# Optimization experiments

Measured on AMD Instinct MI355X. Metric: run time of the kernel, lower is better.

Reference implementation:

```python
import jax, jax.numpy as jnp
import numpy as np

K = 16  # nsample for knn_point

def _bn(x, g, b):
    # inference-mode BatchNorm1d folded to per-channel affine (running stats 0/1)
    return x * g[None, :, None] + b[None, :, None]

def _knn(xyz, k):
    # xyz: [B,3,N] -> idx [B,N,k] of k nearest neighbors (squared L2)
    p = xyz.transpose(0, 2, 1)                                   # [B,N,3]
    sq = jnp.sum(p * p, axis=-1)                                 # [B,N]
    d = sq[:, :, None] + sq[:, None, :] - 2.0 * jnp.einsum('bnc,bmc->bnm', p, p)
    _, idx = jax.lax.top_k(-d, k)
    return idx

def _gather(hT, idx):
    # hT: [B,N,C], idx: [B,N,K] -> [B,N,K,C]
    return jax.vmap(lambda a, i: a[i])(hT, idx)

def setup_inputs():
    key = jax.random.key(0)
    ks = jax.random.split(key, 12)
    B, N, C = 16, 2048, 128
    def w(k, shape, fan):
        return jax.random.normal(k, shape, jnp.float32) * (1.0 / np.sqrt(fan))
    o = jnp.ones; z = jnp.zeros
    return {
        'points': jax.random.normal(ks[0], (B, 6, N), jnp.float32),
        'label': jax.random.uniform(ks[1], (B, 1, 16), jnp.float32),
        'We1': w(ks[2], (C, 6), 6), 'ge1': o(C), 'be1': z(C),
        'We2': w(ks[3], (C, C), C), 'ge2': o(C), 'be2': z(C),
        'W1': w(ks[4], (3, C, C), C), 'g1': o((3, C)), 'b1': z((3, C)),
        'W2': w(ks[5], (3, C, C), C), 'g2': o((3, C)), 'b2': z((3, C)),
        'Wf': w(ks[6], (1024, 3 * C), 3 * C), 'gf': o(1024), 'bf': z(1024),
        'Wl': w(ks[7], (64, 16), 16), 'gl': o(64), 'bl': z(64),
        'Wc1': w(ks[8], (512, 3136), 3136), 'bc1': z(512), 'gc1': o(512), 'bb1': z(512),
        'Wc2': w(ks[9], (256, 512), 512), 'bc2': z(256), 'gc2': o(256), 'bb2': z(256),
        'Wc3': w(ks[10], (50, 256), 256), 'bc3': z(50),
    }

def reference(points, label, We1, ge1, be1, We2, ge2, be2, W1, g1, b1, W2, g2, b2,
              Wf, gf, bf, Wl, gl, bl, Wc1, bc1, gc1, bb1, Wc2, bc2, gc2, bb2, Wc3, bc3):
    B, _, N = points.shape
    x = points[:, :6, :]
    xyz = x[:, :3, :]
    idx = _knn(xyz, K)                                            # [B,N,16]
    # input embedding: two conv1x1 + BN + ReLU
    h = jax.nn.relu(_bn(jnp.einsum('oc,bcn->bon', We1, x), ge1, be1))
    h = jax.nn.relu(_bn(jnp.einsum('oc,bcn->bon', We2, h), ge2, be2))
    xs = []
    for i in range(3):  # PVDSA_Res blocks (simplified: conv-BN-ReLU, kNN max-agg, conv-BN + residual)
        t = jax.nn.relu(_bn(jnp.einsum('oc,bcn->bon', W1[i], h), g1[i], b1[i]))
        nbr = _gather(t.transpose(0, 2, 1), idx)                  # [B,N,K,C]
        m = nbr.max(axis=2).transpose(0, 2, 1)                    # [B,C,N]
        h = jax.nn.relu(_bn(jnp.einsum('oc,bcn->bon', W2[i], m), g2[i], b2[i]) + h)
        xs.append(h)
    xcat = jnp.concatenate(xs, axis=1)                            # [B,384,N]
    xf = jax.nn.leaky_relu(_bn(jnp.einsum('oc,bcn->bon', Wf, xcat), gf, bf), 0.2)  # [B,1024,N]
    x_max = xf.max(axis=-1)                                       # [B,1024]
    x_avg = xf.mean(axis=-1)                                      # [B,1024]
    cls = jnp.broadcast_to(label.transpose(0, 2, 1), (B, 16, N))
    lab = jax.nn.leaky_relu(_bn(jnp.einsum('oc,bcn->bon', Wl, cls), gl, bl), 0.2)  # [B,64,N]
    glob = jnp.concatenate([
        jnp.broadcast_to(x_max[:, :, None], (B, 1024, N)),
        jnp.broadcast_to(x_avg[:, :, None], (B, 1024, N)),
        lab], axis=1)
    xa = jnp.concatenate([xf, glob], axis=1)                      # [B,3136,N]
    c = jax.nn.relu(_bn(jnp.einsum('oc,bcn->bon', Wc1, xa) + bc1[None, :, None], gc1, bb1))
    c = jax.nn.relu(_bn(jnp.einsum('oc,bcn->bon', Wc2, c) + bc2[None, :, None], gc2, bb2))
    out = jnp.einsum('oc,bcn->bon', Wc3, c) + bc3[None, :, None]  # [B,50,N]
    return out
```

## Files before the change

kernel.cpp:

```cpp
#include <hip/hip_runtime.h>
#include <cstdint>
#include <cstddef>

#define DEVINL __device__ __forceinline__

typedef float    f32x4 __attribute__((ext_vector_type(4)));
typedef _Float16 f16x8 __attribute__((ext_vector_type(8)));
typedef _Float16 f16x4 __attribute__((ext_vector_type(4)));
typedef short    s16x8 __attribute__((ext_vector_type(8)));

constexpr int BB = 16, NN = 2048, MM = 32768;

constexpr size_t OFF_WE1 = 0;
constexpr size_t OFF_WE2 = OFF_WE1 + 128 * 64 * 2;
constexpr size_t OFF_W1  = OFF_WE2 + 128 * 128 * 2;
constexpr size_t OFF_W2  = OFF_W1  + 3 * 128 * 128 * 2;
constexpr size_t OFF_WF  = OFF_W2  + 3 * 128 * 128 * 2;
constexpr size_t OFF_WC1 = OFF_WF  + 1024 * 384 * 2;
constexpr size_t OFF_WC2 = OFF_WC1 + 512 * 1024 * 2;
constexpr size_t OFF_WC3 = OFF_WC2 + 256 * 512 * 2;
constexpr size_t OFF_BC2 = OFF_WC3 + 128 * 256 * 2;
constexpr size_t OFF_BC3 = OFF_BC2 + 256 * 4;
constexpr size_t OFF_CVEC= OFF_BC3 + 128 * 4;
constexpr size_t OFF_PMAX= OFF_CVEC+ 16 * 512 * 4;
constexpr size_t OFF_PSUM= OFF_PMAX+ 16 * 16 * 1024 * 4;
constexpr size_t OFF_IDX = OFF_PSUM+ 16 * 16 * 1024 * 4;
constexpr size_t OFF_R1  = 8ull << 20;
constexpr size_t OFF_X0  = OFF_R1;
constexpr size_t OFF_HT  = OFF_R1 + (4ull  << 20);
constexpr size_t OFF_TT  = OFF_R1 + (12ull << 20);
constexpr size_t OFF_MT  = OFF_R1 + (20ull << 20);
constexpr size_t OFF_C1  = OFF_R1;
constexpr size_t OFF_XCAT= OFF_R1 + (32ull << 20);
constexpr size_t OFF_C2  = OFF_XCAT;
constexpr size_t OFF_XF  = OFF_XCAT + (24ull << 20);

__global__ __launch_bounds__(256) void fold_all_kernel(
    const float* We1, const float* ge1, const float* We2, const float* ge2,
    const float* W1,  const float* g1,  const float* W2,  const float* g2,
    const float* Wf,  const float* gf,  const float* Wc1, const float* gc1,
    const float* Wc2, const float* gc2, const float* Wc3,
    const float* gc2b, const float* bc2, const float* bb2, const float* bc3,
    const float* pts, char* ws)
{
    const int bid = blockIdx.x;
    const int tid = threadIdx.x;

    if (bid == 4704) {
        ((float*)(ws + OFF_BC2))[tid] = gc2b[tid] * bc2[tid] + bb2[tid];
        return;
    }
    if (bid == 4705) {
        if (tid < 128) ((float*)(ws + OFF_BC3))[tid] = (tid < 50) ? bc3[tid] : 0.f;
        return;
    }
    if (bid >= 4706) {
        int m = (bid - 4706) * 256 + tid;
        int b = m >> 11, n = m & 2047;
        const float* ps = pts + (size_t)b * 6 * 2048 + n;
        _Float16 tmp[64];
#pragma unroll
        for (int c = 0; c < 64; ++c) tmp[c] = (_Float16)0.f;
#pragma unroll
        for (int c = 0; c < 6; ++c) tmp[c] = (_Float16)ps[(size_t)c << 11];
        _Float16* dst = (_Float16*)(ws + OFF_X0) + (size_t)m * 64;
#pragma unroll
        for (int v = 0; v < 8; ++v) *(f16x8*)(dst + v * 8) = *(const f16x8*)(tmp + v * 8);
        return;
    }

    int id, base;
    if      (bid < 32)   { id = 0;  base = 0;    }
    else if (bid < 96)   { id = 1;  base = 32;   }
    else if (bid < 160)  { id = 2;  base = 96;   }
    else if (bid < 224)  { id = 3;  base = 160;  }
    else if (bid < 288)  { id = 4;  base = 224;  }
    else if (bid < 352)  { id = 5;  base = 288;  }
    else if (bid < 416)  { id = 6;  base = 352;  }
    else if (bid < 480)  { id = 7;  base = 416;  }
    else if (bid < 2016) { id = 8;  base = 480;  }
    else if (bid < 4064) { id = 9;  base = 2016; }
    else if (bid < 4576) { id = 10; base = 4064; }
    else                 { id = 11; base = 4576; }

    const float* src = nullptr; const float* g = nullptr; _Float16* dst = nullptr;
    int O = 0, K = 0, lds = 0, Kp = 0;
    switch (id) {
        case 0:  src = We1; g = ge1; O = 128; K = 6;    lds = 6;    Kp = 64;   dst = (_Float16*)(ws + OFF_WE1); break;
        case 1:  src = We2; g = ge2; O = 128; K = 128;  lds = 128;  Kp = 128;  dst = (_Float16*)(ws + OFF_WE2); break;
        case 2: case 3: case 4: {
            int i = id - 2;
            src = W1 + (size_t)i * 16384; g = g1 + i * 128; O = 128; K = 128; lds = 128; Kp = 128;
            dst = (_Float16*)(ws + OFF_W1) + (size_t)i * 16384; break; }
        case 5: case 6: case 7: {
            int i = id - 5;
            src = W2 + (size_t)i * 16384; g = g2 + i * 128; O = 128; K = 128; lds = 128; Kp = 128;
            dst = (_Float16*)(ws + OFF_W2) + (size_t)i * 16384; break; }
        case 8:  src = Wf;  g = gf;  O = 1024; K = 384;  lds = 384;  Kp = 384;  dst = (_Float16*)(ws + OFF_WF);  break;
        case 9:  src = Wc1; g = gc1; O = 512;  K = 1024; lds = 3136; Kp = 1024; dst = (_Float16*)(ws + OFF_WC1); break;
        case 10: src = Wc2; g = gc2; O = 256;  K = 512;  lds = 512;  Kp = 512;  dst = (_Float16*)(ws + OFF_WC2); break;
        default: src = Wc3; g = nullptr; O = 50; K = 256; lds = 256; Kp = 256;  dst = (_Float16*)(ws + OFF_WC3); break;
    }
    int e = (bid - base) * 256 + tid;
    int o = e / Kp, k = e - o * Kp;
    float v = 0.f;
    if (o < O && k < K) {
        v = src[(size_t)o * lds + k];
        if (g) v *= g[o];
    }
    dst[e] = (_Float16)v;
}

DEVINL float knn_dist(const float4 pq, const float4 pm) {
    float t = pq.x * pm.x;
    t = fmaf(pq.y, pm.y, t);
    t = fmaf(pq.z, pm.z, t);
    return fmaf(-2.f, t, pm.w);
}

#define KNN_DINS(X) do { \
    const float x_ = (X); \
    d15 = __builtin_amdgcn_fmed3f(x_, d14, d15); \
    d14 = __builtin_amdgcn_fmed3f(x_, d13, d14); \
    d13 = __builtin_amdgcn_fmed3f(x_, d12, d13); \
    d12 = __builtin_amdgcn_fmed3f(x_, d11, d12); \
    d11 = __builtin_amdgcn_fmed3f(x_, d10, d11); \
    d10 = __builtin_amdgcn_fmed3f(x_, d9,  d10); \
    d9  = __builtin_amdgcn_fmed3f(x_, d8,  d9);  \
    d8  = __builtin_amdgcn_fmed3f(x_, d7,  d8);  \
    d7  = __builtin_amdgcn_fmed3f(x_, d6,  d7);  \
    d6  = __builtin_amdgcn_fmed3f(x_, d5,  d6);  \
    d5  = __builtin_amdgcn_fmed3f(x_, d4,  d5);  \
    d4  = __builtin_amdgcn_fmed3f(x_, d3,  d4);  \
    d3  = __builtin_amdgcn_fmed3f(x_, d2,  d3);  \
    d2  = __builtin_amdgcn_fmed3f(x_, d1,  d2);  \
    d1  = __builtin_amdgcn_fmed3f(x_, d0,  d1);  \
    d0  = __builtin_amdgcn_fmed3f(x_, -3.4e38f, d0); \
} while (0)

#define KNN_CE(A, B) { const float lo_ = fminf(A, B), hi_ = fmaxf(A, B); A = lo_; B = hi_; }

#define KNN_MERGE(OFF) do { \
    const float n0  = __shfl_xor(d0,  OFF), n1  = __shfl_xor(d1,  OFF), \
                n2  = __shfl_xor(d2,  OFF), n3  = __shfl_xor(d3,  OFF), \
                n4  = __shfl_xor(d4,  OFF), n5  = __shfl_xor(d5,  OFF), \
                n6  = __shfl_xor(d6,  OFF), n7  = __shfl_xor(d7,  OFF), \
                n8  = __shfl_xor(d8,  OFF), n9  = __shfl_xor(d9,  OFF), \
                n10 = __shfl_xor(d10, OFF), n11 = __shfl_xor(d11, OFF), \
                n12 = __shfl_xor(d12, OFF), n13 = __shfl_xor(d13, OFF), \
                n14 = __shfl_xor(d14, OFF), n15 = __shfl_xor(d15, OFF); \
    d0  = fminf(d0,  n15); d1  = fminf(d1,  n14); d2  = fminf(d2,  n13); d3  = fminf(d3,  n12); \
    d4  = fminf(d4,  n11); d5  = fminf(d5,  n10); d6  = fminf(d6,  n9);  d7  = fminf(d7,  n8);  \
    d8  = fminf(d8,  n7);  d9  = fminf(d9,  n6);  d10 = fminf(d10, n5);  d11 = fminf(d11, n4);  \
    d12 = fminf(d12, n3);  d13 = fminf(d13, n2);  d14 = fminf(d14, n1);  d15 = fminf(d15, n0);  \
    KNN_CE(d0, d8)  KNN_CE(d1, d9)  KNN_CE(d2, d10) KNN_CE(d3, d11) \
    KNN_CE(d4, d12) KNN_CE(d5, d13) KNN_CE(d6, d14) KNN_CE(d7, d15) \
    KNN_CE(d0, d4)  KNN_CE(d1, d5)  KNN_CE(d2, d6)  KNN_CE(d3, d7)  \
    KNN_CE(d8, d12) KNN_CE(d9, d13) KNN_CE(d10,d14) KNN_CE(d11,d15) \
    KNN_CE(d0, d2)  KNN_CE(d1, d3)  KNN_CE(d4, d6)  KNN_CE(d5, d7)  \
    KNN_CE(d8, d10) KNN_CE(d9, d11) KNN_CE(d12,d14) KNN_CE(d13,d15) \
    KNN_CE(d0, d1)  KNN_CE(d2, d3)  KNN_CE(d4, d5)  KNN_CE(d6, d7)  \
    KNN_CE(d8, d9)  KNN_CE(d10,d11) KNN_CE(d12,d13) KNN_CE(d14,d15) \
} while (0)

__global__ __launch_bounds__(256) void knn_kernel(const float* __restrict__ pts, int* __restrict__ idxout)
{
    __shared__ float4 P[2048];
    __shared__ unsigned short buf[32][96];
    __shared__ int cnt[32];
    __shared__ int wcnt[32];
    const int tid = threadIdx.x;
    const int b = blockIdx.x;
    const float* pb = pts + (size_t)b * 6 * 2048;
    for (int i = tid; i < 2048; i += 256) {
        float x = pb[i];
        float y = pb[2048 + i];
        float z = pb[4096 + i];
        P[i] = make_float4(x, y, z, x * x + y * y + z * z);
    }
    if (tid < 32) { cnt[tid] = 0; wcnt[tid] = 0; }
    __syncthreads();

    const int p = tid & 7;
    const int g = tid >> 3;
    const int q = blockIdx.y * 32 + g;
    const float4 pq = P[q];

    float d0 = 3.4e38f, d1 = 3.4e38f, d2 = 3.4e38f, d3 = 3.4e38f;
#pragma unroll 4
    for (int it = 0; it < 256; ++it) {
        const float4 pm = P[it * 8 + p];
        const float x = knn_dist(pq, pm);
        d3 = __builtin_amdgcn_fmed3f(x, d2, d3);
        d2 = __builtin_amdgcn_fmed3f(x, d1, d2);
        d1 = __builtin_amdgcn_fmed3f(x, d0, d1);
        d0 = fminf(x, d0);
    }
    float d4 = 3.4e38f, d5 = 3.4e38f, d6 = 3.4e38f, d7 = 3.4e38f,
          d8 = 3.4e38f, d9 = 3.4e38f, d10 = 3.4e38f, d11 = 3.4e38f,
          d12 = 3.4e38f, d13 = 3.4e38f, d14 = 3.4e38f, d15 = 3.4e38f;
    KNN_MERGE(1);
    KNN_MERGE(2);
    KNN_MERGE(4);
    const float tub = d15;

#pragma unroll 4
    for (int it = 0; it < 256; ++it) {
        const int m = it * 8 + p;
        const float d = knn_dist(pq, P[m]);
        if (d <= tub) {
            const int pos = atomicAdd(&cnt[g], 1);
            if (pos < 96) buf[g][pos] = (unsigned short)m;
        }
    }
    int C = cnt[g];
    if (C > 96) C = 96;

    d0 = 3.4e38f; d1 = 3.4e38f; d2 = 3.4e38f; d3 = 3.4e38f;
    d4 = 3.4e38f; d5 = 3.4e38f; d6 = 3.4e38f; d7 = 3.4e38f;
    d8 = 3.4e38f; d9 = 3.4e38f; d10 = 3.4e38f; d11 = 3.4e38f;
    d12 = 3.4e38f; d13 = 3.4e38f; d14 = 3.4e38f; d15 = 3.4e38f;
    for (int j = p; j < C; j += 8) {
        const int m = buf[g][j];
        const float x = knn_dist(pq, P[m]);
        KNN_DINS(x);
    }
    KNN_MERGE(1);
    KNN_MERGE(2);
    KNN_MERGE(4);
    const float t = d15;

    int* op = idxout + (((size_t)(b << 11) + q) << 4);
    for (int j = p; j < C; j += 8) {
        const int m = buf[g][j];
        const float d = knn_dist(pq, P[m]);
        if (d <= t) {
            const int pos = atomicAdd(&wcnt[g], 1);
            if (pos < 16) op[pos] = m;
        }
    }
}

__global__ __launch_bounds__(256) void e12_kernel(
    const _Float16* __restrict__ W1e, const _Float16* __restrict__ W2e,
    const _Float16* __restrict__ X, _Float16* __restrict__ Y,
    const float* __restrict__ b1v, const float* __restrict__ b2v)
{
    __shared__ _Float16 SH[36864];
    _Float16* A1s = SH;
    _Float16* B1s = SH + 8192;
    _Float16* A2s = SH + 12288;
    _Float16* B2s = SH + 28672;

    const int tid = threadIdx.x;
    const int lane = tid & 63, wave = tid >> 6;
    const int r = lane & 15, quad = lane >> 4;
    const int m_blk = blockIdx.x * 64;
    const int oh = (wave >> 1) * 64, mh = (wave & 1) * 32;

    const int srow  = wave * 8 + (lane >> 3);
    const int sslot = lane & 7;

#pragma unroll
    for (int t = 0; t < 4; ++t) {
        const int row = t * 32 + srow;
        const int gk = (sslot ^ (row & 7)) << 3;
        __builtin_amdgcn_global_load_lds(
            (const __attribute__((address_space(1))) unsigned int*)(W1e + (size_t)row * 64 + gk),
            (__attribute__((address_space(3))) unsigned int*)(A1s + t * 2048 + wave * 512),
            16, 0, 0);
    }
#pragma unroll
    for (int t = 0; t < 2; ++t) {
        const int row = t * 32 + srow;
        const int gk = (sslot ^ (row & 7)) << 3;
        __builtin_amdgcn_global_load_lds(
            (const __attribute__((address_space(1))) unsigned int*)(X + (size_t)(m_blk + row) * 64 + gk),
            (__attribute__((address_space(3))) unsigned int*)(B1s + t * 2048 + wave * 512),
            16, 0, 0);
    }
#pragma unroll
    for (int kt = 0; kt < 2; ++kt)
#pragma unroll
        for (int t = 0; t < 4; ++t) {
            const int row = t * 32 + srow;
            const int gk = kt * 64 + ((sslot ^ (row & 7)) << 3);
            __builtin_amdgcn_global_load_lds(
                (const __attribute__((address_space(1))) unsigned int*)(W2e + (size_t)row * 128 + gk),
                (__attribute__((address_space(3))) unsigned int*)(A2s + kt * 8192 + t * 2048 + wave * 512),
                16, 0, 0);
        }

    asm volatile("s_waitcnt vmcnt(8)" ::: "memory");
    __builtin_amdgcn_sched_barrier(0);
    __builtin_amdgcn_s_barrier();
    asm volatile("" ::: "memory");

    f32x4 acc1[4][2];
#pragma unroll
    for (int a = 0; a < 4; ++a)
#pragma unroll
        for (int c = 0; c < 2; ++c) acc1[a][c] = (f32x4){0.f, 0.f, 0.f, 0.f};
#pragma unroll
    for (int ks = 0; ks < 2; ++ks) {
        f16x8 af[4], bf[2];
#pragma unroll
        for (int oi = 0; oi < 4; ++oi) {
            const int row = oh + oi * 16 + r;
            const int slot = (ks * 4 + quad) ^ (row & 7);
            af[oi] = *(const f16x8*)(A1s + row * 64 + slot * 8);
        }
#pragma unroll
        for (int mi = 0; mi < 2; ++mi) {
            const int row = mh + mi * 16 + r;
            const int slot = (ks * 4 + quad) ^ (row & 7);
            bf[mi] = *(const f16x8*)(B1s + row * 64 + slot * 8);
        }
#pragma unroll
        for (int oi = 0; oi < 4; ++oi)
#pragma unroll
            for (int mi = 0; mi < 2; ++mi)
                acc1[oi][mi] = __builtin_amdgcn_mfma_f32_16x16x32_f16(af[oi], bf[mi], acc1[oi][mi], 0, 0, 0);
    }

#pragma unroll
    for (int oi = 0; oi < 4; ++oi) {
        const int ob = oh + oi * 16 + quad * 4;
        const f32x4 bv = *(const f32x4*)(b1v + ob);
        const int kt = ob >> 6, kk = ob & 63;
        const int chunk = kk >> 3, within = kk & 7;
#pragma unroll
        for (int mi = 0; mi < 2; ++mi) {
            const int row = mh + mi * 16 + r;
            f32x4 v = acc1[oi][mi] + bv;
            f16x4 ov;
#pragma unroll
            for (int j = 0; j < 4; ++j) { float x = v[j]; ov[j] = (_Float16)((x > 0.f) ? x : 0.f); }
            *(f16x4*)(B2s + kt * 4096 + row * 64 + ((chunk ^ (row & 7)) << 3) + within) = ov;
        }
    }
    __syncthreads();

    f32x4 acc2[4][2];
#pragma unroll
    for (int a = 0; a < 4; ++a)
#pragma unroll
        for (int c = 0; c < 2; ++c) acc2[a][c] = (f32x4){0.f, 0.f, 0.f, 0.f};
#pragma unroll
    for (int kt = 0; kt < 2; ++kt)
#pragma unroll
        for (int ks = 0; ks < 2; ++ks) {
            f16x8 af[4], bf[2];
#pragma unroll
            for (int oi = 0; oi < 4; ++oi) {
                const int row = oh + oi * 16 + r;
                const int slot = (ks * 4 + quad) ^ (row & 7);
                af[oi] = *(const f16x8*)(A2s + kt * 8192 + row * 64 + slot * 8);
            }
#pragma unroll
            for (int mi = 0; mi < 2; ++mi) {
                const int row = mh + mi * 16 + r;
                const int slot = (ks * 4 + quad) ^ (row & 7);
                bf[mi] = *(const f16x8*)(B2s + kt * 4096 + row * 64 + slot * 8);
            }
#pragma unroll
            for (int oi = 0; oi < 4; ++oi)
#pragma unroll
                for (int mi = 0; mi < 2; ++mi)
                    acc2[oi][mi] = __builtin_amdgcn_mfma_f32_16x16x32_f16(af[oi], bf[mi], acc2[oi][mi], 0, 0, 0);
        }
    __syncthreads();

    _Float16* OT = SH;
#pragma unroll
    for (int oi = 0; oi < 4; ++oi) {
        const int ol = oh + oi * 16 + quad * 4;
        const f32x4 bv = *(const f32x4*)(b2v + ol);
#pragma unroll
        for (int mi = 0; mi < 2; ++mi) {
            const int row = mh + mi * 16 + r;
            f32x4 v = acc2[oi][mi] + bv;
            f16x4 ov;
#pragma unroll
            for (int j = 0; j < 4; ++j) { float x = v[j]; ov[j] = (_Float16)((x > 0.f) ? x : 0.f); }
            const int s = ((ol >> 2) ^ (row & 31)) << 2;
            *(f16x4*)(OT + row * 128 + s) = ov;
        }
    }
    __syncthreads();
#pragma unroll
    for (int it2 = 0; it2 < 4; ++it2) {
        const int row = it2 * 16 + (tid >> 4);
        const int c = tid & 15;
        const int s0 = ((c * 2) ^ (row & 31)) << 2;
        const int s1 = ((c * 2 + 1) ^ (row & 31)) << 2;
        f16x4 a  = *(const f16x4*)(OT + row * 128 + s0);
        f16x4 b2 = *(const f16x4*)(OT + row * 128 + s1);
        f16x8 o8;
        o8[0] = a[0]; o8[1] = a[1]; o8[2] = a[2]; o8[3] = a[3];
        o8[4] = b2[0]; o8[5] = b2[1]; o8[6] = b2[2]; o8[7] = b2[3];
        *(f16x8*)(Y + (size_t)(m_blk + row) * 128 + c * 8) = o8;
    }
}

template<bool HAS_G2>
__global__ __launch_bounds__(256) void pairg_kernel(
    const _Float16* __restrict__ Wa, const _Float16* __restrict__ Wb,
    const short* __restrict__ T, const int* __restrict__ idxp,
    const _Float16* __restrict__ Res,
    _Float16* __restrict__ Y1, _Float16* __restrict__ Y2,
    const float* __restrict__ ba, const float* __restrict__ bb,
    int ldR, int roff, int yoff1)
{
    __shared__ _Float16 SH[32768];
    _Float16* Aa  = SH;
    _Float16* Bm  = SH + 16384;
    _Float16* By1 = SH + 24576;
    _Float16* Ab  = SH;
    _Float16* OT2 = SH + 16384;

    const int tid = threadIdx.x;
    const int lane = tid & 63, wave = tid >> 6;
    const int r = lane & 15, quad = lane >> 4;
    const int m_blk = blockIdx.x * 64;
    const int oh = (wave >> 1) * 64, mh = (wave & 1) * 32;

    const int srow  = wave * 8 + (lane >> 3);
    const int sslot = lane & 7;

#pragma unroll
    for (int kt = 0; kt < 2; ++kt)
#pragma unroll
        for (int t = 0; t < 4; ++t) {
            const int row = t * 32 + srow;
            const int gk = kt * 64 + ((sslot ^ (row & 7)) << 3);
            __builtin_amdgcn_global_load_lds(
                (const __attribute__((address_space(1))) unsigned int*)(Wa + (size_t)row * 128 + gk),
                (__attribute__((address_space(3))) unsigned int*)(Aa + kt * 8192 + t * 2048 + wave * 512),
                16, 0, 0);
        }

    {
        const int l = tid & 15;
        const int kt = l >> 3, cc = l & 7;
#pragma unroll
        for (int it = 0; it < 4; ++it) {
            const int row = it * 16 + (tid >> 4);
            const int gm = m_blk + row;
            const int b = gm >> 11;
            const int* ip = idxp + (size_t)gm * 16;
            size_t rr = (size_t)((b << 11) + ip[0]);
            s16x8 cur = *(const s16x8*)(T + rr * 128 + l * 8);
            unsigned short best[8];
#pragma unroll
            for (int e = 0; e < 8; ++e) best[e] = (unsigned short)cur[e];
#pragma unroll
            for (int j = 1; j < 16; ++j) {
                rr = (size_t)((b << 11) + ip[j]);
                s16x8 v = *(const s16x8*)(T + rr * 128 + l * 8);
#pragma unroll
                for (int e = 0; e < 8; ++e) {
                    unsigned short u = (unsigned short)v[e];
                    if (u > best[e]) best[e] = u;
                }
            }
            s16x8 ov;
#pragma unroll
            for (int e = 0; e < 8; ++e) ov[e] = (short)best[e];
            *(s16x8*)((short*)Bm + kt * 4096 + row * 64 + ((cc ^ (row & 7)) << 3)) = ov;
        }
    }
    __syncthreads();

    f32x4 acc1[4][2];
#pragma unroll
    for (int a = 0; a < 4; ++a)
#pragma unroll
        for (int c = 0; c < 2; ++c) acc1[a][c] = (f32x4){0.f, 0.f, 0.f, 0.f};
#pragma unroll
    for (int kt = 0; kt < 2; ++kt)
#pragma unroll
        for (int ks = 0; ks < 2; ++ks) {
            f16x8 af[4], bf[2];
#pragma unroll
            for (int oi = 0; oi < 4; ++oi) {
                const int row = oh + oi * 16 + r;
                const int slot = (ks * 4 + quad) ^ (row & 7);
                af[oi] = *(const f16x8*)(Aa + kt * 8192 + row * 64 + slot * 8);
            }
#pragma unroll
            for (int mi = 0; mi < 2; ++mi) {
                const int row = mh + mi * 16 + r;
                const int slot = (ks * 4 + quad) ^ (row & 7);
                bf[mi] = *(const f16x8*)(Bm + kt * 4096 + row * 64 + slot * 8);
            }
#pragma unroll
            for (int oi = 0; oi < 4; ++oi)
#pragma unroll
                for (int mi = 0; mi < 2; ++mi)
                    acc1[oi][mi] = __builtin_amdgcn_mfma_f32_16x16x32_f16(af[oi], bf[mi], acc1[oi][mi], 0, 0, 0);
        }
    __syncthreads();

    if constexpr (HAS_G2) {
#pragma unroll
        for (int kt = 0; kt < 2; ++kt)
#pragma unroll
            for (int t = 0; t < 4; ++t) {
                const int row = t * 32 + srow;
                const int gk = kt * 64 + ((sslot ^ (row & 7)) << 3);
                __builtin_amdgcn_global_load_lds(
                    (const __attribute__((address_space(1))) unsigned int*)(Wb + (size_t)row * 128 + gk),
                    (__attribute__((address_space(3))) unsigned int*)(Ab + kt * 8192 + t * 2048 + wave * 512),
                    16, 0, 0);
            }
    }

#pragma unroll
    for (int oi = 0; oi < 4; ++oi) {
        const int ol = oh + oi * 16 + quad * 4;
        const f32x4 bv = *(const f32x4*)(ba + ol);
        const int kt = ol >> 6, kk = ol & 63;
        const int chunk = kk >> 3, within = kk & 7;
#pragma unroll
        for (int mi = 0; mi < 2; ++mi) {
            const int row = mh + mi * 16 + r;
            f32x4 v = acc1[oi][mi] + bv;
            f16x4 rr = *(const f16x4*)(Res + (size_t)(m_blk + row) * ldR + roff + ol);
#pragma unroll
            for (int j = 0; j < 4; ++j) v[j] += (float)rr[j];
            f16x4 ov;
#pragma unroll
            for (int j = 0; j < 4; ++j) { float x = v[j]; ov[j] = (_Float16)((x > 0.f) ? x : 0.f); }
            *(f16x4*)(By1 + kt * 4096 + row * 64 + ((chunk ^ (row & 7)) << 3) + within) = ov;
        }
    }
    __syncthreads();

#pragma unroll
    for (int it = 0; it < 4; ++it) {
        const int g = it * 256 + tid;
        const int row = g >> 4, c = g & 15;
        const int kt = c >> 3, cc = c & 7;
        f16x8 o8 = *(const f16x8*)(By1 + kt * 4096 + row * 64 + ((cc ^ (row & 7)) << 3));
        *(f16x8*)(Y1 + (size_t)(m_blk + row) * 384 + yoff1 + c * 8) = o8;
    }

    if constexpr (HAS_G2) {
        f32x4 acc2[4][2];
#pragma unroll
        for (int a = 0; a < 4; ++a)
#pragma unroll
            for (int c = 0; c < 2; ++c) acc2[a][c] = (f32x4){0.f, 0.f, 0.f, 0.f};
#pragma unroll
        for (int kt = 0; kt < 2; ++kt)
#pragma unroll
            for (int ks = 0; ks < 2; ++ks) {
                f16x8 af[4], bf[2];
#pragma unroll
                for (int oi = 0; oi < 4; ++oi) {
                    const int row = oh + oi * 16 + r;
                    const int slot = (ks * 4 + quad) ^ (row & 7);
                    af[oi] = *(const f16x8*)(Ab + kt * 8192 + row * 64 + slot * 8);
                }
#pragma unroll
                for (int mi = 0; mi < 2; ++mi) {
                    const int row = mh + mi * 16 + r;
                    const int slot = (ks * 4 + quad) ^ (row & 7);
                    bf[mi] = *(const f16x8*)(By1 + kt * 4096 + row * 64 + slot * 8);
                }
#pragma unroll
                for (int oi = 0; oi < 4; ++oi)
#pragma unroll
                    for (int mi = 0; mi < 2; ++mi)
                        acc2[oi][mi] = __builtin_amdgcn_mfma_f32_16x16x32_f16(af[oi], bf[mi], acc2[oi][mi], 0, 0, 0);
            }

#pragma unroll
        for (int oi = 0; oi < 4; ++oi) {
            const int ol = oh + oi * 16 + quad * 4;
            const f32x4 bv = *(const f32x4*)(bb + ol);
#pragma unroll
            for (int mi = 0; mi < 2; ++mi) {
                const int row = mh + mi * 16 + r;
                f32x4 v = acc2[oi][mi] + bv;
                f16x4 ov;
#pragma unroll
                for (int j = 0; j < 4; ++j) { float x = v[j]; ov[j] = (_Float16)((x > 0.f) ? x : 0.f); }
                const int s = ((ol >> 2) ^ (row & 31)) << 2;
                *(f16x4*)(OT2 + row * 128 + s) = ov;
            }
        }
        __syncthreads();
#pragma unroll
        for (int it2 = 0; it2 < 4; ++it2) {
            const int row = it2 * 16 + (tid >> 4);
            const int c = tid & 15;
            const int s0 = ((c * 2) ^ (row & 31)) << 2;
            const int s1 = ((c * 2 + 1) ^ (row & 31)) << 2;
            f16x4 a  = *(const f16x4*)(OT2 + row * 128 + s0);
            f16x4 b2 = *(const f16x4*)(OT2 + row * 128 + s1);
            f16x8 o8;
            o8[0] = a[0]; o8[1] = a[1]; o8[2] = a[2]; o8[3] = a[3];
            o8[4] = b2[0]; o8[5] = b2[1]; o8[6] = b2[2]; o8[7] = b2[3];
            *(f16x8*)(Y2 + (size_t)(m_blk + row) * 128 + c * 8) = o8;
        }
    }
}

__global__ __launch_bounds__(512, 2) void gemm256(
    const _Float16* __restrict__ W, const _Float16* __restrict__ X,
    _Float16* __restrict__ Y, const float* __restrict__ bias,
    int Kp, int ldX, int ldY, int Opad, int act, int biasPerBatch,
    float* __restrict__ pmax, float* __restrict__ psum)
{
    constexpr int ASZ = 256 * 64;
    __shared__ _Float16 SH[65536];
    const int tid  = threadIdx.x;
    const int lane = tid & 63, wave = tid >> 6;
    const int r = lane & 15, quad = lane >> 4;
    const int wo = wave & 3, wm = wave >> 2;
    const int m_blk = blockIdx.x * 256, o_blk = blockIdx.y * 256;
    const int nt = Kp >> 6;

    f32x4 acc[4][8];
#pragma unroll
    for (int a = 0; a < 4; ++a)
#pragma unroll
        for (int c = 0; c < 8; ++c) acc[a][c] = (f32x4){0.f, 0.f, 0.f, 0.f};

    const int srow  = wave * 8 + (lane >> 3);
    const int sslot = lane & 7;

    auto STAGE = [&](int bufi, int k0) {
        _Float16* As = SH + bufi * (2 * ASZ);
        _Float16* Bs = As + ASZ;
#pragma unroll
        for (int t = 0; t < 4; ++t) {
            const int rowA = t * 64 + srow;
            const int gk = k0 + ((sslot ^ (rowA & 7)) << 3);
            const _Float16* gA = W + (size_t)(o_blk + rowA) * Kp + gk;
            __builtin_amdgcn_global_load_lds(
                (const __attribute__((address_space(1))) unsigned int*)gA,
                (__attribute__((address_space(3))) unsigned int*)(As + t * 4096 + wave * 512),
                16, 0, 0);
        }
#pragma unroll
        for (int t = 0; t < 4; ++t) {
            const int rowB = t * 64 + srow;
            const int gk = k0 + ((sslot ^ (rowB & 7)) << 3);
            const _Float16* gB = X + (size_t)(m_blk + rowB) * ldX + gk;
            __builtin_amdgcn_global_load_lds(
                (const __attribute__((address_space(1))) unsigned int*)gB,
                (__attribute__((address_space(3))) unsigned int*)(Bs + t * 4096 + wave * 512),
                16, 0, 0);
        }
    };

    STAGE(0, 0);
    int cur = 0;
    for (int t = 0; t < nt; ++t) {
        if (t + 1 < nt) {
            STAGE(cur ^ 1, (t + 1) << 6);
            asm volatile("s_waitcnt vmcnt(8)" ::: "memory");
        } else {
            asm volatile("s_waitcnt vmcnt(0)" ::: "memory");
        }
        __builtin_amdgcn_sched_barrier(0);
        __builtin_amdgcn_s_barrier();
        asm volatile("" ::: "memory");

        const _Float16* As = SH + cur * (2 * ASZ);
        const _Float16* Bs = As + ASZ;
        __builtin_amdgcn_s_setprio(1);
#pragma unroll
        for (int ks = 0; ks < 2; ++ks) {
            f16x8 af[4], bf[8];
#pragma unroll
            for (int oi = 0; oi < 4; ++oi) {
                const int row = (wo << 6) + (oi << 4) + r;
                const int slot = (ks * 4 + quad) ^ (row & 7);
                af[oi] = *(const f16x8*)(As + row * 64 + slot * 8);
            }
#pragma unroll
            for (int mi = 0; mi < 8; ++mi) {
                const int row = (wm << 7) + (mi << 4) + r;
                const int slot = (ks * 4 + quad) ^ (row & 7);
                bf[mi] = *(const f16x8*)(Bs + row * 64 + slot * 8);
            }
#pragma unroll
            for (int oi = 0; oi < 4; ++oi)
#pragma unroll
                for (int mi = 0; mi < 8; ++mi)
                    acc[oi][mi] = __builtin_amdgcn_mfma_f32_16x16x32_f16(af[oi], bf[mi], acc[oi][mi], 0, 0, 0);
        }
        __builtin_amdgcn_s_setprio(0);
        asm volatile("" ::: "memory");
        __builtin_amdgcn_s_barrier();
        cur ^= 1;
    }
    __syncthreads();

    const int bb = biasPerBatch ? (m_blk >> 11) * Opad : 0;
    _Float16* OT = SH;
#pragma unroll
    for (int oi = 0; oi < 4; ++oi) {
        const int ol = (wo << 6) + (oi << 4) + (quad << 2);
        const f32x4 bv = *(const f32x4*)(bias + bb + o_blk + ol);
#pragma unroll
        for (int mi = 0; mi < 8; ++mi) {
            const int row = (wm << 7) + (mi << 4) + r;
            f32x4 v = acc[oi][mi] + bv;
            f16x4 ov;
#pragma unroll
            for (int j = 0; j < 4; ++j) {
                float x = v[j];
                if (act == 1)      x = (x > 0.f) ? x : 0.0f;
                else if (act == 2) x = (x > 0.f) ? x : 0.2f * x;
                ov[j] = (_Float16)x;
            }
            const int s = (ol >> 2) ^ (row & 31);
            *(f16x4*)(OT + row * 256 + s * 4) = ov;
        }
    }
    __syncthreads();
#pragma unroll
    for (int p2 = 0; p2 < 16; ++p2) {
        const int g = (p2 << 9) + tid;
        const int row = g >> 5, c = g & 31;
        const int s0 = ((c << 1)) ^ (row & 31);
        const int s1 = ((c << 1) | 1) ^ (row & 31);
        f16x4 a  = *(const f16x4*)(OT + row * 256 + s0 * 4);
        f16x4 b2 = *(const f16x4*)(OT + row * 256 + s1 * 4);
        f16x8 o8;
        o8[0] = a[0]; o8[1] = a[1]; o8[2] = a[2]; o8[3] = a[3];
        o8[4] = b2[0]; o8[5] = b2[1]; o8[6] = b2[2]; o8[7] = b2[3];
        *(f16x8*)(Y + (size_t)(m_blk + row) * ldY + o_blk + (c << 3)) = o8;
    }

    if (pmax) {
        const int cg = tid & 63, h8 = tid >> 6;
        float mx0 = -3.4e38f, mx1 = -3.4e38f, mx2 = -3.4e38f, mx3 = -3.4e38f;
        float sm0 = 0.f, sm1 = 0.f, sm2 = 0.f, sm3 = 0.f;
#pragma unroll
        for (int rr = 0; rr < 32; ++rr) {
            const int row = (h8 << 5) + rr;
            const f16x4 v = *(const f16x4*)(OT + row * 256 + ((cg ^ (row & 31)) << 2));
            const float x0 = (float)v[0], x1 = (float)v[1], x2 = (float)v[2], x3 = (float)v[3];
            mx0 = fmaxf(mx0, x0); sm0 += x0;
            mx1 = fmaxf(mx1, x1); sm1 += x1;
            mx2 = fmaxf(mx2, x2); sm2 += x2;
            mx3 = fmaxf(mx3, x3); sm3 += x3;
        }
        __syncthreads();
        float* PR = (float*)SH;
        float* pw = PR + (size_t)(((h8 << 8) + (cg << 2)) << 1);
        pw[0] = mx0; pw[1] = sm0; pw[2] = mx1; pw[3] = sm1;
        pw[4] = mx2; pw[5] = sm2; pw[6] = mx3; pw[7] = sm3;
        __syncthreads();
        if (tid < 256) {
            float M = -3.4e38f, S = 0.f;
#pragma unroll
            for (int h2 = 0; h2 < 8; ++h2) {
                M = fmaxf(M, PR[(size_t)(((h2 << 8) + tid) << 1)]);
                S += PR[(size_t)(((h2 << 8) + tid) << 1) + 1];
            }
            const int b2 = m_blk >> 11, mt = (m_blk >> 8) & 7;
            pmax[((size_t)((b2 << 3) + mt) << 10) + o_blk + tid] = M;
            psum[((size_t)((b2 << 3) + mt) << 10) + o_blk + tid] = S;
        }
    }
}

template<int TM>
__global__ __launch_bounds__(256) void gemm_tile(
    const _Float16* __restrict__ W, const _Float16* __restrict__ X,
    _Float16* __restrict__ Y, float* __restrict__ Y32,
    const float* __restrict__ bias, const _Float16* __restrict__ Res,
    int Kp, int ldX, int xoff, int ldY, int yoff, int Opad,
    int act, int biasPerBatch, int ldR, int roff, int Olimit)
{
    constexpr int MI = TM / 32;
    constexpr int ASZ = 128 * 64;
    constexpr int BSZ = TM * 64;
    __shared__ _Float16 SH[2 * (ASZ + BSZ)];

    const int tid  = threadIdx.x;
    const int lane = tid & 63, wave = tid >> 6;
    const int r = lane & 15, quad = lane >> 4;
    const int m_blk = blockIdx.x * TM, o_blk = blockIdx.y * 128;
    const int oh = (wave >> 1) * 64, mh = (wave & 1) * (TM / 2);

    f32x4 acc[4][MI];
#pragma unroll
    for (int a = 0; a < 4; ++a)
#pragma unroll
        for (int c = 0; c < MI; ++c) acc[a][c] = (f32x4){0.f, 0.f, 0.f, 0.f};

    const int srow  = wave * 8 + (lane >> 3);
    const int sslot = lane & 7;

    auto STAGE = [&](int bufi, int k0) {
        _Float16* As = SH + bufi * (ASZ + BSZ);
        _Float16* Bs = As + ASZ;
#pragma unroll
        for (int t = 0; t < 4; ++t) {
            const int rowA = t * 32 + srow;
            const int gk = k0 + ((sslot ^ (rowA & 7)) << 3);
            const _Float16* gA = W + (size_t)(o_blk + rowA) * Kp + gk;
            __builtin_amdgcn_global_load_lds(
                (const __attribute__((address_space(1))) unsigned int*)gA,
                (__attribute__((address_space(3))) unsigned int*)(As + t * 2048 + wave * 512),
                16, 0, 0);
        }
#pragma unroll
        for (int t = 0; t < TM / 32; ++t) {
            const int rowB = t * 32 + srow;
            const int gk = k0 + ((sslot ^ (rowB & 7)) << 3);
            const _Float16* gB = X + (size_t)(m_blk + rowB) * ldX + xoff + gk;
            __builtin_amdgcn_global_load_lds(
                (const __attribute__((address_space(1))) unsigned int*)gB,
                (__attribute__((address_space(3))) unsigned int*)(Bs + t * 2048 + wave * 512),
                16, 0, 0);
        }
    };

    const int nt = Kp >> 6;
    STAGE(0, 0);
    int cur = 0;
    for (int t = 0; t < nt; ++t) {
        if (t + 1 < nt) {
            STAGE(cur ^ 1, (t + 1) << 6);
            if constexpr (TM == 128) asm volatile("s_waitcnt vmcnt(8)" ::: "memory");
            else                     asm volatile("s_waitcnt vmcnt(6)" ::: "memory");
        } else {
            asm volatile("s_waitcnt vmcnt(0)" ::: "memory");
        }
        __builtin_amdgcn_sched_barrier(0);
        __builtin_amdgcn_s_barrier();
        asm volatile("" ::: "memory");

        const _Float16* As = SH + cur * (ASZ + BSZ);
        const _Float16* Bs = As + ASZ;
        __builtin_amdgcn_s_setprio(1);
#pragma unroll
        for (int ks = 0; ks < 2; ++ks) {
            f16x8 af[4], bf[MI];
#pragma unroll
            for (int oi = 0; oi < 4; ++oi) {
                const int row = oh + oi * 16 + r;
                const int slot = (ks * 4 + quad) ^ (row & 7);
                af[oi] = *(const f16x8*)(As + row * 64 + slot * 8);
            }
#pragma unroll
            for (int mi = 0; mi < MI; ++mi) {
                const int row = mh + mi * 16 + r;
                const int slot = (ks * 4 + quad) ^ (row & 7);
                bf[mi] = *(const f16x8*)(Bs + row * 64 + slot * 8);
            }
#pragma unroll
            for (int oi = 0; oi < 4; ++oi)
#pragma unroll
                for (int mi = 0; mi < MI; ++mi)
                    acc[oi][mi] = __builtin_amdgcn_mfma_f32_16x16x32_f16(af[oi], bf[mi], acc[oi][mi], 0, 0, 0);
        }
        __builtin_amdgcn_s_setprio(0);
        asm volatile("" ::: "memory");
        __builtin_amdgcn_s_barrier();
        cur ^= 1;
    }

    const int bb = biasPerBatch ? (m_blk >> 11) * Opad : 0;
    __syncthreads();

    if (Y32) {
#pragma unroll
        for (int oi = 0; oi < 4; ++oi) {
            const int og = o_blk + oh + oi * 16 + quad * 4;
            const f32x4 bv = *(const f32x4*)(bias + bb + og);
#pragma unroll
            for (int mi = 0; mi < MI; ++mi) {
                const int m = m_blk + mh + mi * 16 + r;
                const int bidx = m >> 11, n = m & 2047;
                f32x4 v = acc[oi][mi] + bv;
#pragma unroll
                for (int j = 0; j < 4; ++j) {
                    float x = v[j];
                    if (act == 1)      x = (x > 0.f) ? x : 0.0f;
                    else if (act == 2) x = (x > 0.f) ? x : 0.2f * x;
                    const int o = og + j;
                    if (o < Olimit)
                        Y32[((size_t)(bidx * 50 + o) << 11) + n] = x;
                }
            }
        }
        return;
    }

    _Float16* OT = SH;
#pragma unroll
    for (int oi = 0; oi < 4; ++oi) {
        const int ol = oh + oi * 16 + quad * 4;
        const f32x4 bv = *(const f32x4*)(bias + bb + o_blk + ol);
#pragma unroll
        for (int mi = 0; mi < MI; ++mi) {
            const int row = mh + mi * 16 + r;
            f32x4 v = acc[oi][mi] + bv;
            if (Res) {
                f16x4 rr = *(const f16x4*)(Res + (size_t)(m_blk + row) * ldR + roff + o_blk + ol);
#pragma unroll
                for (int j = 0; j < 4; ++j) v[j] += (float)rr[j];
            }
            f16x4 ov;
#pragma unroll
            for (int j = 0; j < 4; ++j) {
                float x = v[j];
                if (act == 1)      x = (x > 0.f) ? x : 0.0f;
                else if (act == 2) x = (x > 0.f) ? x : 0.2f * x;
                ov[j] = (_Float16)x;
            }
            const int s = ((ol >> 2) ^ (row & 31)) << 2;
            *(f16x4*)(OT + row * 128 + s) = ov;
        }
    }
    __syncthreads();
#pragma unroll
    for (int it2 = 0; it2 < TM / 16; ++it2) {
        const int row = it2 * 16 + (tid >> 4);
        const int c = tid & 15;
        const int s0 = ((c * 2) ^ (row & 31)) << 2;
        const int s1 = ((c * 2 + 1) ^ (row & 31)) << 2;
        f16x4 a = *(const f16x4*)(OT + row * 128 + s0);
        f16x4 b2 = *(const f16x4*)(OT + row * 128 + s1);
        f16x8 o8;
        o8[0] = a[0]; o8[1] = a[1]; o8[2] = a[2]; o8[3] = a[3];
        o8[4] = b2[0]; o8[5] = b2[1]; o8[6] = b2[2]; o8[7] = b2[3];
        *(f16x8*)(Y + (size_t)(m_blk + row) * ldY + yoff + o_blk + c * 8) = o8;
    }
}

__global__ __launch_bounds__(256) void cvec_kernel(
    const float* __restrict__ label, const float* __restrict__ Wl, const float* __restrict__ gl, const float* __restrict__ bl,
    const float* __restrict__ Wc1, const float* __restrict__ bc1, const float* __restrict__ gc1, const float* __restrict__ bb1,
    const float* __restrict__ pmax, const float* __restrict__ psum, float* __restrict__ cvec)
{
    __shared__ float v[2112];
    __shared__ float red[256];
    const int b = blockIdx.x, og = blockIdx.y, tid = threadIdx.x;
    for (int i = tid; i < 1024; i += 256) {
        float mx = -3.4e38f, sm = 0.f;
#pragma unroll
        for (int c = 0; c < 8; ++c) {
            mx = fmaxf(mx, pmax[((size_t)(b * 8 + c) << 10) + i]);
            sm += psum[((size_t)(b * 8 + c) << 10) + i];
        }
        v[i] = mx;
        v[1024 + i] = sm * (1.f / 2048.f);
    }
    if (tid < 64) {
        float s = 0.f;
        for (int i = 0; i < 16; ++i) s += Wl[tid * 16 + i] * label[b * 16 + i];
        s = gl[tid] * s + bl[tid];
        v[2048 + tid] = (s > 0.f) ? s : 0.2f * s;
    }
    __syncthreads();
    const int o = og * 64 + (tid >> 2), part = tid & 3;
    const float* wrow = Wc1 + (size_t)o * 3136 + 1024 + part * 528;
    float s = 0.f;
    for (int j = 0; j < 528; ++j) s += wrow[j] * v[part * 528 + j];
    red[tid] = s;
    __syncthreads();
    if (part == 0) {
        float tot = red[tid] + red[tid + 1] + red[tid + 2] + red[tid + 3];
        cvec[((size_t)b << 9) + o] = gc1[o] * (tot + bc1[o]) + bb1[o];
    }
}

extern "C" void kernel_launch(void* const* d_in, const int* in_sizes, int n_in,
                              void* d_out, int out_size, void* d_ws, size_t ws_size,
                              hipStream_t stream)
{
    (void)in_sizes; (void)n_in; (void)out_size; (void)ws_size;
    const float* points = (const float*)d_in[0];
    const float* label  = (const float*)d_in[1];
    const float* We1 = (const float*)d_in[2];
    const float* ge1 = (const float*)d_in[3];
    const float* be1 = (const float*)d_in[4];
    const float* We2 = (const float*)d_in[5];
    const float* ge2 = (const float*)d_in[6];
    const float* be2 = (const float*)d_in[7];
    const float* W1  = (const float*)d_in[8];
    const float* g1  = (const float*)d_in[9];
    const float* b1  = (const float*)d_in[10];
    const float* W2  = (const float*)d_in[11];
    const float* g2  = (const float*)d_in[12];
    const float* b2  = (const float*)d_in[13];
    const float* Wf  = (const float*)d_in[14];
    const float* gf  = (const float*)d_in[15];
    const float* bfv = (const float*)d_in[16];
    const float* Wl  = (const float*)d_in[17];
    const float* gl  = (const float*)d_in[18];
    const float* bl  = (const float*)d_in[19];
    const float* Wc1 = (const float*)d_in[20];
    const float* bc1 = (const float*)d_in[21];
    const float* gc1 = (const float*)d_in[22];
    const float* bb1 = (const float*)d_in[23];
    const float* Wc2 = (const float*)d_in[24];
    const float* bc2 = (const float*)d_in[25];
    const float* gc2 = (const float*)d_in[26];
    const float* bb2 = (const float*)d_in[27];
    const float* Wc3 = (const float*)d_in[28];
    const float* bc3 = (const float*)d_in[29];

    char* ws = (char*)d_ws;
    _Float16* hT  = (_Float16*)(ws + OFF_HT);
    _Float16* tT  = (_Float16*)(ws + OFF_TT);
    _Float16* tT2 = (_Float16*)(ws + OFF_MT);
    _Float16* xct = (_Float16*)(ws + OFF_XCAT);
    _Float16* xf  = (_Float16*)(ws + OFF_XF);
    _Float16* c1  = (_Float16*)(ws + OFF_C1);
    _Float16* c2  = (_Float16*)(ws + OFF_C2);
    int*      idx = (int*)     (ws + OFF_IDX);
    _Float16* x0  = (_Float16*)(ws + OFF_X0);

    _Float16* wE1 = (_Float16*)(ws + OFF_WE1);
    _Float16* wE2 = (_Float16*)(ws + OFF_WE2);
    _Float16* w1f = (_Float16*)(ws + OFF_W1);
    _Float16* w2f = (_Float16*)(ws + OFF_W2);
    _Float16* wF  = (_Float16*)(ws + OFF_WF);
    _Float16* wC1 = (_Float16*)(ws + OFF_WC1);
    _Float16* wC2 = (_Float16*)(ws + OFF_WC2);
    _Float16* wC3 = (_Float16*)(ws + OFF_WC3);
    float* bC2 = (float*)(ws + OFF_BC2);
    float* bC3 = (float*)(ws + OFF_BC3);
    float* cv  = (float*)(ws + OFF_CVEC);
    float* pmx = (float*)(ws + OFF_PMAX);
    float* psm = (float*)(ws + OFF_PSUM);

    fold_all_kernel<<<dim3(4834), 256, 0, stream>>>(We1, ge1, We2, ge2, W1, g1, W2, g2,
                                                    Wf, gf, Wc1, gc1, Wc2, gc2, Wc3,
                                                    gc2, bc2, bb2, bc3, points, ws);
    knn_kernel<<<dim3(BB, NN / 32), 256, 0, stream>>>(points, idx);

    e12_kernel<<<dim3(512), 256, 0, stream>>>(wE1, wE2, x0, hT, be1, be2);

    gemm_tile<64><<<dim3(512, 1), 256, 0, stream>>>(w1f, hT, tT, nullptr, b1, nullptr,
                                                    128, 128, 0, 128, 0, 128, 1, 0, 0, 0, 128);

    pairg_kernel<true><<<dim3(512), 256, 0, stream>>>(w2f, w1f + 16384, (const short*)tT, idx, hT,
                                                      xct, tT2, b2, b1 + 128, 128, 0, 0);

    pairg_kernel<true><<<dim3(512), 256, 0, stream>>>(w2f + 16384, w1f + 2 * 16384, (const short*)tT2, idx, xct,
                                                      xct, tT, b2 + 128, b1 + 256, 384, 0, 128);

    pairg_kernel<false><<<dim3(512), 256, 0, stream>>>(w2f + 2 * 16384, nullptr, (const short*)tT, idx, xct,
                                                       xct, nullptr, b2 + 256, nullptr, 384, 128, 256);

    gemm256<<<dim3(128, 4), 512, 0, stream>>>(wF, xct, xf, bfv, 384, 384, 1024, 1024, 2, 0, pmx, psm);

    cvec_kernel<<<dim3(BB, 8), 256, 0, stream>>>(label, Wl, gl, bl, Wc1, bc1, gc1, bb1, pmx, psm, cv);

    gemm256<<<dim3(128, 2), 512, 0, stream>>>(wC1, xf, c1, cv, 1024, 1024, 512, 512, 1, 1, nullptr, nullptr);

    gemm_tile<128><<<dim3(256, 2), 256, 0, stream>>>(wC2, c1, c2, nullptr, bC2, nullptr, 512, 512, 0, 256, 0, 256, 1, 0, 0, 0, 256);
    gemm_tile<128><<<dim3(256, 1), 256, 0, stream>>>(wC3, c2, nullptr, (float*)d_out, bC3, nullptr, 256, 256, 0, 0, 0, 128, 0, 0, 0, 0, 50);
}
```

Baseline: 366.2 us.

## Fuse final two pointwise conv GEMMs into one kernel keeping intermediate in LDS

Replaces the separate Wc2 (512->256, ReLU) and Wc3 (256->50) GEMM launches with a single kernel that computes a 64-point tile of the 256-channel hidden activation, stores it in shared memory as fp16, and immediately multiplies it by Wc3 to write the fp32 output. This removes the global round trip of the c2 intermediate and one kernel launch. In exchange, each block reloads the full Wc2 and Wc3 weights, uses a smaller 64-wide point tile with no double buffering, and wastes MFMA work padding 50 output channels to 128.

```diff
diff --git a/kernel.cpp b/kernel.cpp
--- a/kernel.cpp
+++ b/kernel.cpp
@@ -32,7 +32,6 @@
 constexpr size_t OFF_MT  = OFF_R1 + (20ull << 20);
 constexpr size_t OFF_C1  = OFF_R1;
 constexpr size_t OFF_XCAT= OFF_R1 + (32ull << 20);
-constexpr size_t OFF_C2  = OFF_XCAT;
 constexpr size_t OFF_XF  = OFF_XCAT + (24ull << 20);
 
 __global__ __launch_bounds__(256) void fold_all_kernel(
@@ -604,6 +603,175 @@
             o8[0] = a[0]; o8[1] = a[1]; o8[2] = a[2]; o8[3] = a[3];
             o8[4] = b2[0]; o8[5] = b2[1]; o8[6] = b2[2]; o8[7] = b2[3];
             *(f16x8*)(Y2 + (size_t)(m_blk + row) * 128 + c * 8) = o8;
+        }
+    }
+}
+
+__global__ __launch_bounds__(256) void c2c3_kernel(
+    const _Float16* __restrict__ W2c, const _Float16* __restrict__ W3c,
+    const _Float16* __restrict__ X, float* __restrict__ Y32,
+    const float* __restrict__ b2v, const float* __restrict__ b3v)
+{
+    __shared__ _Float16 SH[36864];
+    _Float16* As = SH;
+    _Float16* Bs = SH + 16384;
+    _Float16* Y1 = SH + 20480;
+
+    const int tid = threadIdx.x;
+    const int lane = tid & 63, w = tid >> 6;
+    const int r = lane & 15, quad = lane >> 4;
+    const int m_blk = blockIdx.x * 64;
+
+    const int srow  = w * 8 + (lane >> 3);
+    const int sslot = lane & 7;
+
+    f32x4 acc1[4][4];
+#pragma unroll
+    for (int a = 0; a < 4; ++a)
+#pragma unroll
+        for (int c = 0; c < 4; ++c) acc1[a][c] = (f32x4){0.f, 0.f, 0.f, 0.f};
+
+    for (int kt8 = 0; kt8 < 8; ++kt8) {
+        const int k0 = kt8 << 6;
+        __syncthreads();
+#pragma unroll
+        for (int t = 0; t < 8; ++t) {
+            const int row = t * 32 + srow;
+            const int gk = k0 + ((sslot ^ (row & 7)) << 3);
+            __builtin_amdgcn_global_load_lds(
+                (const __attribute__((address_space(1))) unsigned int*)(W2c + (size_t)row * 512 + gk),
+                (__attribute__((address_space(3))) unsigned int*)(As + t * 2048 + w * 512),
+                16, 0, 0);
+        }
+#pragma unroll
+        for (int t = 0; t < 2; ++t) {
+            const int row = t * 32 + srow;
+            const int gk = k0 + ((sslot ^ (row & 7)) << 3);
+            __builtin_amdgcn_global_load_lds(
+                (const __attribute__((address_space(1))) unsigned int*)(X + (size_t)(m_blk + row) * 512 + gk),
+                (__attribute__((address_space(3))) unsigned int*)(Bs + t * 2048 + w * 512),
+                16, 0, 0);
+        }
+        __syncthreads();
+#pragma unroll
+        for (int ks = 0; ks < 2; ++ks) {
+            f16x8 af[4], bf[4];
+#pragma unroll
+            for (int oi = 0; oi < 4; ++oi) {
+                const int row = w * 64 + oi * 16 + r;
+                const int slot = (ks * 4 + quad) ^ (row & 7);
+                af[oi] = *(const f16x8*)(As + row * 64 + slot * 8);
+            }
+#pragma unroll
+            for (int mi = 0; mi < 4; ++mi) {
+                const int row = mi * 16 + r;
+                const int slot = (ks * 4 + quad) ^ (row & 7);
+                bf[mi] = *(const f16x8*)(Bs + row * 64 + slot * 8);
+            }
+#pragma unroll
+            for (int oi = 0; oi < 4; ++oi)
+#pragma unroll
+                for (int mi = 0; mi < 4; ++mi)
+                    acc1[oi][mi] = __builtin_amdgcn_mfma_f32_16x16x32_f16(af[oi], bf[mi], acc1[oi][mi], 0, 0, 0);
+        }
+    }
+    __syncthreads();
+
+#pragma unroll
+    for (int kk2 = 0; kk2 < 2; ++kk2)
+#pragma unroll
+        for (int t = 0; t < 4; ++t) {
+            const int row = t * 32 + srow;
+            const int gk = (kk2 << 6) + ((sslot ^ (row & 7)) << 3);
+            __builtin_amdgcn_global_load_lds(
+                (const __attribute__((address_space(1))) unsigned int*)(W3c + (size_t)row * 256 + gk),
+                (__attribute__((address_space(3))) unsigned int*)(As + kk2 * 8192 + t * 2048 + w * 512),
+                16, 0, 0);
+        }
+
+#pragma unroll
+    for (int oi = 0; oi < 4; ++oi) {
+        const int ol = w * 64 + oi * 16 + quad * 4;
+        const f32x4 bv = *(const f32x4*)(b2v + ol);
+        const int kk = ol & 63;
+        const int chunk = kk >> 3, within = kk & 7;
+#pragma unroll
+        for (int mi = 0; mi < 4; ++mi) {
+            const int row = mi * 16 + r;
+            f32x4 v = acc1[oi][mi] + bv;
+            f16x4 ov;
+#pragma unroll
+            for (int j = 0; j < 4; ++j) { float x = v[j]; ov[j] = (_Float16)((x > 0.f) ? x : 0.f); }
+            *(f16x4*)(Y1 + w * 4096 + row * 64 + ((chunk ^ (row & 7)) << 3) + within) = ov;
+        }
+    }
+    __syncthreads();
+
+    f32x4 acc2[2][4];
+#pragma unroll
+    for (int a = 0; a < 2; ++a)
+#pragma unroll
+        for (int c = 0; c < 4; ++c) acc2[a][c] = (f32x4){0.f, 0.f, 0.f, 0.f};
+
+#pragma unroll
+    for (int h = 0; h < 2; ++h) {
+        if (h == 1) {
+            __syncthreads();
+#pragma unroll
+            for (int kk2 = 0; kk2 < 2; ++kk2)
+#pragma unroll
+                for (int t = 0; t < 4; ++t) {
+                    const int row = t * 32 + srow;
+                    const int gk = ((2 + kk2) << 6) + ((sslot ^ (row & 7)) << 3);
+                    __builtin_amdgcn_global_load_lds(
+                        (const __attribute__((address_space(1))) unsigned int*)(W3c + (size_t)row * 256 + gk),
+                        (__attribute__((address_space(3))) unsigned int*)(As + kk2 * 8192 + t * 2048 + w * 512),
+                        16, 0, 0);
+                }
+            __syncthreads();
+        }
+#pragma unroll
+        for (int kk2 = 0; kk2 < 2; ++kk2) {
+            const int kt = h * 2 + kk2;
+#pragma unroll
+            for (int ks = 0; ks < 2; ++ks) {
+                f16x8 af2[2], bf2[4];
+#pragma unroll
+                for (int oi2 = 0; oi2 < 2; ++oi2) {
+                    const int row = w * 32 + oi2 * 16 + r;
+                    const int slot = (ks * 4 + quad) ^ (row & 7);
+                    af2[oi2] = *(const f16x8*)(As + kk2 * 8192 + row * 64 + slot * 8);
+                }
+#pragma unroll
+                for (int mi = 0; mi < 4; ++mi) {
+                    const int row = mi * 16 + r;
+                    const int slot = (ks * 4 + quad) ^ (row & 7);
+                    bf2[mi] = *(const f16x8*)(Y1 + kt * 4096 + row * 64 + slot * 8);
+                }
+#pragma unroll
+                for (int oi2 = 0; oi2 < 2; ++oi2)
+#pragma unroll
+                    for (int mi = 0; mi < 4; ++mi)
+                        acc2[oi2][mi] = __builtin_amdgcn_mfma_f32_16x16x32_f16(af2[oi2], bf2[mi], acc2[oi2][mi], 0, 0, 0);
+            }
+        }
+    }
+
+#pragma unroll
+    for (int oi2 = 0; oi2 < 2; ++oi2) {
+        const int og = w * 32 + oi2 * 16 + quad * 4;
+        const f32x4 bv = *(const f32x4*)(b3v + og);
+#pragma unroll
+        for (int mi = 0; mi < 4; ++mi) {
+            const int m = m_blk + mi * 16 + r;
+            const int bidx = m >> 11, n = m & 2047;
+            f32x4 v = acc2[oi2][mi] + bv;
+#pragma unroll
+            for (int j = 0; j < 4; ++j) {
+                const int o = og + j;
+                if (o < 50)
+                    Y32[((size_t)(bidx * 50 + o) << 11) + n] = v[j];
+            }
         }
     }
 }
@@ -1019,7 +1187,6 @@
     _Float16* xct = (_Float16*)(ws + OFF_XCAT);
     _Float16* xf  = (_Float16*)(ws + OFF_XF);
     _Float16* c1  = (_Float16*)(ws + OFF_C1);
-    _Float16* c2  = (_Float16*)(ws + OFF_C2);
     int*      idx = (int*)     (ws + OFF_IDX);
     _Float16* x0  = (_Float16*)(ws + OFF_X0);
 
@@ -1062,6 +1229,5 @@
 
     gemm256<<<dim3(128, 2), 512, 0, stream>>>(wC1, xf, c1, cv, 1024, 1024, 512, 512, 1, 1, nullptr, nullptr);
 
-    gemm_tile<128><<<dim3(256, 2), 256, 0, stream>>>(wC2, c1, c2, nullptr, bC2, nullptr, 512, 512, 0, 256, 0, 256, 1, 0, 0, 0, 256);
-    gemm_tile<128><<<dim3(256, 1), 256, 0, stream>>>(wC3, c2, nullptr, (float*)d_out, bC3, nullptr, 256, 256, 0, 0, 0, 128, 0, 0, 0, 0, 50);
+    c2c3_kernel<<<dim3(512), 256, 0, stream>>>(wC2, wC3, c1, (float*)d_out, bC2, bC3);
 }
```

Measured after the change: 366.7 us. About the same (+0.1%).
